# Kernel tuning notes

Measured on AMD Instinct MI355X. Metric: run time of the kernel, lower is better.

## Reference

```python
import jax, jax.numpy as jnp
import numpy as np

B, N, D = 8, 8192, 3

def setup_inputs() -> dict:
    key = jax.random.key(0)
    k1, k2 = jax.random.split(key)
    adv_pc = jax.random.normal(k1, (B, N, D), dtype=jnp.float32)
    ori_pc = jax.random.normal(k2, (B, N, D), dtype=jnp.float32)
    weights = jnp.ones((B,), dtype=jnp.float32)
    return {"adv_pc": adv_pc, "ori_pc": ori_pc, "weights": weights}

def _batch_pairwise_dist(x, y):
    # x: [B, Nx, D], y: [B, Ny, D] -> P: [B, Nx, Ny]
    rx = jnp.sum(x * x, axis=-1)                      # [B, Nx]
    ry = jnp.sum(y * y, axis=-1)                      # [B, Ny]
    zz = jnp.einsum('bnd,bmd->bnm', x, y)             # [B, Nx, Ny]
    return rx[:, :, None] + ry[:, None, :] - 2.0 * zz

def reference(adv_pc, ori_pc, weights):
    # chamfer(preds=adv_pc, gts=ori_pc): P = pairwise(ori, adv) -> [B, N_ori, N_adv]
    P = _batch_pairwise_dist(ori_pc, adv_pc)
    loss1 = jnp.mean(jnp.min(P, axis=1), axis=1)      # adv2ori: for each adv pt, nearest ori
    # method == 'adv2ori' -> loss = loss1
    loss = loss1 * weights
    return jnp.mean(loss)
```

## Files before the change

kernel.cpp:

```cpp
#include <hip/hip_runtime.h>
#include <float.h>

#define NB 8
#define NPTS 8192
#define TOTAL (NB * NPTS)
#define BLK 256
#define WAVES 4
#define ADV_PER_WAVE 64
#define ADV_PER_BLOCK (WAVES * ADV_PER_WAVE)
#define ADV_BLOCKS (TOTAL / ADV_PER_BLOCK)
#define OSPLIT 4
#define OSLICE (NPTS / OSPLIT)
#define OCH 1024
#define NCHUNK (OSLICE / OCH)
#define REC_SHORTS 16
#define GRID_MAIN (ADV_BLOCKS * OSPLIT)
#define BF16_ONE 0x3F80

typedef short short8 __attribute__((ext_vector_type(8)));
typedef float floatx16 __attribute__((ext_vector_type(16)));

__device__ __forceinline__ unsigned short f2bf(float f) {
    unsigned int u = __float_as_uint(f);
    return (unsigned short)((u + 0x7FFFu + ((u >> 16) & 1u)) >> 16);
}
__device__ __forceinline__ float bf2f(unsigned short h) {
    return __uint_as_float(((unsigned int)h) << 16);
}

__global__ __launch_bounds__(BLK) void build_recs(const float* __restrict__ ori,
                                                  unsigned short* __restrict__ recs) {
    int g = blockIdx.x * BLK + threadIdx.x;
    float x = ori[3 * g + 0], y = ori[3 * g + 1], z = ori[3 * g + 2];
    unsigned short hx = f2bf(x), hy = f2bf(y), hz = f2bf(z);
    unsigned short lx = f2bf(x - bf2f(hx));
    unsigned short ly = f2bf(y - bf2f(hy));
    unsigned short lz = f2bf(z - bf2f(hz));
    float ro = fmaf(x, x, fmaf(y, y, z * z));
    unsigned short rh = f2bf(ro), rl = f2bf(ro - bf2f(rh));
    __align__(16) unsigned short r[16] = {hx, hy, hz, lx, ly, lz, hx, hy,
                                          hz, rh, rl, 0, 0, 0, 0, 0};
    float4* dst = (float4*)(recs + (size_t)g * REC_SHORTS);
    dst[0] = ((float4*)r)[0];
    dst[1] = ((float4*)r)[1];
}

__device__ __forceinline__ float fold16(floatx16 d, float um) {
    float m0 = fminf(d[0], d[1]),   m1 = fminf(d[2], d[3]);
    float m2 = fminf(d[4], d[5]),   m3 = fminf(d[6], d[7]);
    float m4 = fminf(d[8], d[9]),   m5 = fminf(d[10], d[11]);
    float m6 = fminf(d[12], d[13]), m7 = fminf(d[14], d[15]);
    float n0 = fminf(m0, m1), n1 = fminf(m2, m3);
    float n2 = fminf(m4, m5), n3 = fminf(m6, m7);
    return fminf(um, fminf(fminf(n0, n1), fminf(n2, n3)));
}

__global__ __launch_bounds__(BLK, 4) void chamfer_mfma(const float* __restrict__ adv,
                                                       const unsigned short* __restrict__ recs,
                                                       float* __restrict__ partial) {
    __shared__ __align__(16) unsigned short lrec[OCH * REC_SHORTS];
    const int tid = threadIdx.x;
    const int wave = tid >> 6, lane = tid & 63;
    const int n32 = lane & 31, half = lane >> 5;
    const int advBlk = blockIdx.x >> 2;
    const int split = blockIdx.x & 3;
    const int b = advBlk >> 5;
    const int advLocal = (advBlk & 31) * ADV_PER_BLOCK + wave * ADV_PER_WAVE;

    short8 bfr[2];
    float ra[2], um[2] = {FLT_MAX, FLT_MAX};
    const float* advb = adv + (size_t)b * NPTS * 3;
#pragma unroll
    for (int g2 = 0; g2 < 2; g2++) {
        int j = advLocal + g2 * 32 + n32;
        float x = advb[3 * j + 0], y = advb[3 * j + 1], z = advb[3 * j + 2];
        ra[g2] = fmaf(x, x, fmaf(y, y, z * z));
        unsigned short hx = f2bf(x), hy = f2bf(y), hz = f2bf(z);
        float fhx = bf2f(hx), fhy = bf2f(hy), fhz = bf2f(hz);
        unsigned short nhx = f2bf(-2.0f * fhx), nhy = f2bf(-2.0f * fhy), nhz = f2bf(-2.0f * fhz);
        unsigned short nlx = f2bf(-2.0f * bf2f(f2bf(x - fhx)));
        unsigned short nly = f2bf(-2.0f * bf2f(f2bf(y - fhy)));
        unsigned short nlz = f2bf(-2.0f * bf2f(f2bf(z - fhz)));
        __align__(16) unsigned short e[8] = {0, 0, 0, 0, 0, 0, 0, 0};
        if (half == 0) {
            e[0] = nhx; e[1] = nhy; e[2] = nhz;
            e[3] = nhx; e[4] = nhy; e[5] = nhz;
            e[6] = nlx; e[7] = nly;
        } else {
            e[0] = nlz; e[1] = BF16_ONE; e[2] = BF16_ONE;
        }
        bfr[g2] = *(short8*)e;
    }

    const floatx16 zero = {0.f, 0.f, 0.f, 0.f, 0.f, 0.f, 0.f, 0.f,
                           0.f, 0.f, 0.f, 0.f, 0.f, 0.f, 0.f, 0.f};
    const int lsh = n32 * REC_SHORTS + half * 8;
    const float4* gsrc = (const float4*)recs;

    for (int c = 0; c < NCHUNK; c++) {
        __syncthreads();
        const float4* src = gsrc + (size_t)(b * NPTS + split * OSLICE + c * OCH) * 2;
#pragma unroll
        for (int i = 0; i < (OCH * 2) / BLK; i++)
            ((float4*)lrec)[i * BLK + tid] = src[i * BLK + tid];
        __syncthreads();

#pragma unroll 4
        for (int t = 0; t < OCH / 32; t++) {
            short8 af = *(const short8*)&lrec[t * 32 * REC_SHORTS + lsh];
            floatx16 d0 = __builtin_amdgcn_mfma_f32_32x32x16_bf16(af, bfr[0], zero, 0, 0, 0);
            floatx16 d1 = __builtin_amdgcn_mfma_f32_32x32x16_bf16(af, bfr[1], zero, 0, 0, 0);
            um[0] = fold16(d0, um[0]);
            um[1] = fold16(d1, um[1]);
        }
    }

#pragma unroll
    for (int g2 = 0; g2 < 2; g2++) {
        float v = fminf(um[g2], __shfl_xor(um[g2], 32, 64));
        if (half == 0) {
            int col = b * NPTS + advLocal + g2 * 32 + n32;
            partial[(size_t)split * TOTAL + col] = ra[g2] + v;
        }
    }
}

__global__ __launch_bounds__(BLK) void reduce_mins(const float* __restrict__ partial,
                                                   const float* __restrict__ w,
                                                   float* __restrict__ out) {
    int g = blockIdx.x * BLK + threadIdx.x;
    float m = partial[g];
#pragma unroll
    for (int s = 1; s < OSPLIT; s++) m = fminf(m, partial[(size_t)s * TOTAL + g]);
    float v = m * w[g >> 13];
    __shared__ float red[BLK];
    red[threadIdx.x] = v;
    __syncthreads();
    for (int s = BLK / 2; s > 0; s >>= 1) {
        if (threadIdx.x < s) red[threadIdx.x] += red[threadIdx.x + s];
        __syncthreads();
    }
    if (threadIdx.x == 0) atomicAdd(out, red[0] * (1.0f / (float)TOTAL));
}

extern "C" void kernel_launch(void* const* d_in, const int* in_sizes, int n_in,
                              void* d_out, int out_size, void* d_ws, size_t ws_size,
                              hipStream_t stream) {
    const float* adv = (const float*)d_in[0];
    const float* ori = (const float*)d_in[1];
    const float* w   = (const float*)d_in[2];
    float* out = (float*)d_out;

    unsigned short* recs = (unsigned short*)d_ws;
    float* partial = (float*)((char*)d_ws + (size_t)TOTAL * REC_SHORTS * 2);

    hipMemsetAsync(out, 0, sizeof(float), stream);
    hipLaunchKernelGGL(build_recs, dim3(TOTAL / BLK), dim3(BLK), 0, stream, ori, recs);
    hipLaunchKernelGGL(chamfer_mfma, dim3(GRID_MAIN), dim3(BLK), 0, stream, adv, recs, partial);
    hipLaunchKernelGGL(reduce_mins, dim3(TOTAL / BLK), dim3(BLK), 0, stream, partial, w, out);
}
```

Measured before the change: 92.39 us.

## Fuse ori record build into chamfer kernel and widen adv reuse per wave

```diff
diff --git a/kernel.cpp b/kernel.cpp
--- a/kernel.cpp
+++ b/kernel.cpp
@@ -6,13 +6,12 @@
 #define TOTAL (NB * NPTS)
 #define BLK 256
 #define WAVES 4
-#define ADV_PER_WAVE 64
+#define ADV_PER_WAVE 128
+#define GROUPS 4
 #define ADV_PER_BLOCK (WAVES * ADV_PER_WAVE)
 #define ADV_BLOCKS (TOTAL / ADV_PER_BLOCK)
-#define OSPLIT 4
+#define OSPLIT 8
 #define OSLICE (NPTS / OSPLIT)
-#define OCH 1024
-#define NCHUNK (OSLICE / OCH)
 #define REC_SHORTS 16
 #define GRID_MAIN (ADV_BLOCKS * OSPLIT)
 #define BF16_ONE 0x3F80
@@ -27,54 +26,64 @@
 __device__ __forceinline__ float bf2f(unsigned short h) {
     return __uint_as_float(((unsigned int)h) << 16);
 }
-
-__global__ __launch_bounds__(BLK) void build_recs(const float* __restrict__ ori,
-                                                  unsigned short* __restrict__ recs) {
-    int g = blockIdx.x * BLK + threadIdx.x;
-    float x = ori[3 * g + 0], y = ori[3 * g + 1], z = ori[3 * g + 2];
-    unsigned short hx = f2bf(x), hy = f2bf(y), hz = f2bf(z);
-    unsigned short lx = f2bf(x - bf2f(hx));
-    unsigned short ly = f2bf(y - bf2f(hy));
-    unsigned short lz = f2bf(z - bf2f(hz));
-    float ro = fmaf(x, x, fmaf(y, y, z * z));
-    unsigned short rh = f2bf(ro), rl = f2bf(ro - bf2f(rh));
-    __align__(16) unsigned short r[16] = {hx, hy, hz, lx, ly, lz, hx, hy,
-                                          hz, rh, rl, 0, 0, 0, 0, 0};
-    float4* dst = (float4*)(recs + (size_t)g * REC_SHORTS);
-    dst[0] = ((float4*)r)[0];
-    dst[1] = ((float4*)r)[1];
+__device__ __forceinline__ float min3(float a, float b, float c) {
+    return fminf(fminf(a, b), c);
 }
-
 __device__ __forceinline__ float fold16(floatx16 d, float um) {
-    float m0 = fminf(d[0], d[1]),   m1 = fminf(d[2], d[3]);
-    float m2 = fminf(d[4], d[5]),   m3 = fminf(d[6], d[7]);
-    float m4 = fminf(d[8], d[9]),   m5 = fminf(d[10], d[11]);
-    float m6 = fminf(d[12], d[13]), m7 = fminf(d[14], d[15]);
-    float n0 = fminf(m0, m1), n1 = fminf(m2, m3);
-    float n2 = fminf(m4, m5), n3 = fminf(m6, m7);
-    return fminf(um, fminf(fminf(n0, n1), fminf(n2, n3)));
+    float t0 = min3(d[0], d[1], d[2]);
+    float t1 = min3(d[3], d[4], d[5]);
+    float t2 = min3(d[6], d[7], d[8]);
+    float t3 = min3(d[9], d[10], d[11]);
+    float t4 = min3(d[12], d[13], d[14]);
+    float t5 = min3(t0, t1, d[15]);
+    float t6 = min3(t2, t3, t4);
+    return min3(t5, t6, um);
 }
 
 __global__ __launch_bounds__(BLK, 4) void chamfer_mfma(const float* __restrict__ adv,
-                                                       const unsigned short* __restrict__ recs,
+                                                       const float* __restrict__ ori,
                                                        float* __restrict__ partial) {
-    __shared__ __align__(16) unsigned short lrec[OCH * REC_SHORTS];
+    __shared__ __align__(16) unsigned short lrec[OSLICE * REC_SHORTS];
     const int tid = threadIdx.x;
     const int wave = tid >> 6, lane = tid & 63;
     const int n32 = lane & 31, half = lane >> 5;
-    const int advBlk = blockIdx.x >> 2;
-    const int split = blockIdx.x & 3;
-    const int b = advBlk >> 5;
-    const int advLocal = (advBlk & 31) * ADV_PER_BLOCK + wave * ADV_PER_WAVE;
+    const int advBlk = blockIdx.x >> 3;
+    const int split = blockIdx.x & 7;
+    const int b = advBlk >> 4;
+    const int advLocal = (advBlk & 15) * ADV_PER_BLOCK + wave * ADV_PER_WAVE;
 
-    short8 bfr[2];
-    float ra[2], um[2] = {FLT_MAX, FLT_MAX};
+    {
+        const float4* op = (const float4*)(ori + (size_t)(b * NPTS + split * OSLICE) * 3);
+        float4 f0 = op[tid * 3 + 0], f1 = op[tid * 3 + 1], f2 = op[tid * 3 + 2];
+        float px[4] = {f0.x, f0.w, f1.z, f2.y};
+        float py[4] = {f0.y, f1.x, f1.w, f2.z};
+        float pz[4] = {f0.z, f1.y, f2.x, f2.w};
+#pragma unroll
+        for (int r = 0; r < 4; r++) {
+            float x = px[r], y = py[r], z = pz[r];
+            unsigned short hx = f2bf(x), hy = f2bf(y), hz = f2bf(z);
+            unsigned short lx = f2bf(x - bf2f(hx));
+            unsigned short ly = f2bf(y - bf2f(hy));
+            unsigned short lz = f2bf(z - bf2f(hz));
+            float ro = fmaf(x, x, fmaf(y, y, z * z));
+            unsigned short rh = f2bf(ro), rl = f2bf(ro - bf2f(rh));
+            __align__(16) unsigned short rec[16] = {hx, hy, hz, lx, ly, lz, hx, hy,
+                                                    hz, rh, rl, 0, 0, 0, 0, 0};
+            float4* dst = (float4*)&lrec[(tid * 4 + r) * REC_SHORTS];
+            dst[0] = ((float4*)rec)[0];
+            dst[1] = ((float4*)rec)[1];
+        }
+    }
+
+    short8 bfr[GROUPS];
+    float ra[GROUPS], um[GROUPS];
     const float* advb = adv + (size_t)b * NPTS * 3;
 #pragma unroll
-    for (int g2 = 0; g2 < 2; g2++) {
-        int j = advLocal + g2 * 32 + n32;
+    for (int g = 0; g < GROUPS; g++) {
+        int j = advLocal + g * 32 + n32;
         float x = advb[3 * j + 0], y = advb[3 * j + 1], z = advb[3 * j + 2];
-        ra[g2] = fmaf(x, x, fmaf(y, y, z * z));
+        ra[g] = fmaf(x, x, fmaf(y, y, z * z));
+        um[g] = FLT_MAX;
         unsigned short hx = f2bf(x), hy = f2bf(y), hz = f2bf(z);
         float fhx = bf2f(hx), fhy = bf2f(hy), fhz = bf2f(hz);
         unsigned short nhx = f2bf(-2.0f * fhx), nhy = f2bf(-2.0f * fhy), nhz = f2bf(-2.0f * fhz);
@@ -89,38 +98,30 @@
         } else {
             e[0] = nlz; e[1] = BF16_ONE; e[2] = BF16_ONE;
         }
-        bfr[g2] = *(short8*)e;
+        bfr[g] = *(short8*)e;
     }
+    __syncthreads();
 
     const floatx16 zero = {0.f, 0.f, 0.f, 0.f, 0.f, 0.f, 0.f, 0.f,
                            0.f, 0.f, 0.f, 0.f, 0.f, 0.f, 0.f, 0.f};
     const int lsh = n32 * REC_SHORTS + half * 8;
-    const float4* gsrc = (const float4*)recs;
-
-    for (int c = 0; c < NCHUNK; c++) {
-        __syncthreads();
-        const float4* src = gsrc + (size_t)(b * NPTS + split * OSLICE + c * OCH) * 2;
-#pragma unroll
-        for (int i = 0; i < (OCH * 2) / BLK; i++)
-            ((float4*)lrec)[i * BLK + tid] = src[i * BLK + tid];
-        __syncthreads();
 
 #pragma unroll 4
-        for (int t = 0; t < OCH / 32; t++) {
-            short8 af = *(const short8*)&lrec[t * 32 * REC_SHORTS + lsh];
-            floatx16 d0 = __builtin_amdgcn_mfma_f32_32x32x16_bf16(af, bfr[0], zero, 0, 0, 0);
-            floatx16 d1 = __builtin_amdgcn_mfma_f32_32x32x16_bf16(af, bfr[1], zero, 0, 0, 0);
-            um[0] = fold16(d0, um[0]);
-            um[1] = fold16(d1, um[1]);
+    for (int t = 0; t < OSLICE / 32; t++) {
+        short8 af = *(const short8*)&lrec[t * 32 * REC_SHORTS + lsh];
+#pragma unroll
+        for (int g = 0; g < GROUPS; g++) {
+            floatx16 d = __builtin_amdgcn_mfma_f32_32x32x16_bf16(af, bfr[g], zero, 0, 0, 0);
+            um[g] = fold16(d, um[g]);
         }
     }
 
 #pragma unroll
-    for (int g2 = 0; g2 < 2; g2++) {
-        float v = fminf(um[g2], __shfl_xor(um[g2], 32, 64));
+    for (int g = 0; g < GROUPS; g++) {
+        float v = fminf(um[g], __shfl_xor(um[g], 32, 64));
         if (half == 0) {
-            int col = b * NPTS + advLocal + g2 * 32 + n32;
-            partial[(size_t)split * TOTAL + col] = ra[g2] + v;
+            int col = b * NPTS + advLocal + g * 32 + n32;
+            partial[(size_t)split * TOTAL + col] = ra[g] + v;
         }
     }
 }
@@ -150,12 +151,11 @@
     const float* ori = (const float*)d_in[1];
     const float* w   = (const float*)d_in[2];
     float* out = (float*)d_out;
-
-    unsigned short* recs = (unsigned short*)d_ws;
-    float* partial = (float*)((char*)d_ws + (size_t)TOTAL * REC_SHORTS * 2);
+    float* partial = (float*)d_ws;
 
     hipMemsetAsync(out, 0, sizeof(float), stream);
-    hipLaunchKernelGGL(build_recs, dim3(TOTAL / BLK), dim3(BLK), 0, stream, ori, recs);
-    hipLaunchKernelGGL(chamfer_mfma, dim3(GRID_MAIN), dim3(BLK), 0, stream, adv, recs, partial);
-    hipLaunchKernelGGL(reduce_mins, dim3(TOTAL / BLK), dim3(BLK), 0, stream, partial, w, out);
+    hipLaunchKernelGGL(chamfer_mfma, dim3(GRID_MAIN), dim3(BLK), 0, stream,
+                       adv, ori, partial);
+    hipLaunchKernelGGL(reduce_mins, dim3(TOTAL / BLK), dim3(BLK), 0, stream,
+                       partial, w, out);
 }
```

After: 80.66 us. -12.7%, faster.
